# Kernel tuning notes

Hardware: AMD Instinct MI355X
Metric: run time of the kernel (lower is better)

## Reference

```python
import jax, jax.numpy as jnp
import numpy as np

EPS = 1e-12


def _l2norm(v):
    return v / (jnp.linalg.norm(v) + EPS)


def _sn(W, u):
    """One-step power-iteration spectral normalization (torch spectral_norm, 1x1 conv weight).
    W: (out, in), u: (out,). u/v are treated as buffers (no grad)."""
    Wm = W.reshape(W.shape[0], -1)
    v = _l2norm(Wm.T @ u)
    u2 = _l2norm(Wm @ v)
    u2 = jax.lax.stop_gradient(u2)
    v = jax.lax.stop_gradient(v)
    sigma = u2 @ (Wm @ v)
    return W / sigma


def _maxpool2(x):
    # 2x2 max pool, stride 2, NCHW
    N, C, H, W = x.shape
    return x.reshape(N, C, H // 2, 2, W // 2, 2).max(axis=(3, 5))


def setup_inputs() -> dict:
    key = jax.random.key(0)
    ks = jax.random.split(key, 10)
    N, C, H, W = 16, 256, 64, 64
    s = 0.05  # keep logits moderate
    return {
        "x": jax.random.normal(ks[0], (N, C, H, W), dtype=jnp.float32),
        "Wt": jax.random.normal(ks[1], (C >> 3, C), dtype=jnp.float32) * s,
        "Wp": jax.random.normal(ks[2], (C >> 3, C), dtype=jnp.float32) * s,
        "Wg": jax.random.normal(ks[3], (C >> 1, C), dtype=jnp.float32) * s,
        "Wo": jax.random.normal(ks[4], (C, C >> 1), dtype=jnp.float32) * s,
        "ut": jax.random.normal(ks[5], (C >> 3,), dtype=jnp.float32),
        "up": jax.random.normal(ks[6], (C >> 3,), dtype=jnp.float32),
        "ug": jax.random.normal(ks[7], (C >> 1,), dtype=jnp.float32),
        "uo": jax.random.normal(ks[8], (C,), dtype=jnp.float32),
        "gamma": jnp.float32(0.1),  # nonzero so attention branch is exercised
    }


def reference(x, Wt, Wp, Wg, Wo, ut, up, ug, uo, gamma):
    N, C, H, W = x.shape
    L = H * W          # location_num
    Ld = L // 4        # downsampled_num
    # 1x1 convs as channel einsums with spectrally-normalized weights
    theta = jnp.einsum('oc,nchw->nohw', _sn(Wt, ut), x).reshape(N, C >> 3, L)
    phi = _maxpool2(jnp.einsum('oc,nchw->nohw', _sn(Wp, up), x)).reshape(N, C >> 3, Ld)
    attn = jax.nn.softmax(jnp.einsum('ncl,ncm->nlm', theta, phi), axis=-1)  # (N, L, Ld)
    g = _maxpool2(jnp.einsum('oc,nchw->nohw', _sn(Wg, ug), x)).reshape(N, C >> 1, Ld)
    attn_g = jnp.einsum('ncm,nlm->ncl', g, attn).reshape(N, C >> 1, H, W)
    attn_g = jnp.einsum('oc,nchw->nohw', _sn(Wo, uo), attn_g)
    return x + gamma * attn_g
```

## Files before the change

kernel.cpp:

```cpp
#include <hip/hip_runtime.h>
#include <math.h>

#define EPS 1e-12f

typedef unsigned short ushort_t;
typedef __attribute__((ext_vector_type(8))) short short8;
typedef __attribute__((ext_vector_type(4))) float f32x4;
typedef __attribute__((ext_vector_type(4))) unsigned short ushort4v;
typedef __attribute__((ext_vector_type(2))) unsigned int uint2v;
typedef __attribute__((ext_vector_type(4))) unsigned int uint32x4;

#define WS_WB_F 0
#define WS_WO_F 24576
#define WS_TH_F 40960
#define WS_PH_F 1089536
#define WS_G_F  1351680

__device__ __forceinline__ ushort_t f2bf(float f) {
  unsigned int u = __float_as_uint(f);
  u += 0x7fffu + ((u >> 16) & 1u);
  return (ushort_t)(u >> 16);
}
__device__ __forceinline__ float bf2f(ushort_t u) {
  return __uint_as_float(((unsigned int)u) << 16);
}
__device__ __forceinline__ unsigned int pack_bfrh(float lo, float hi) {
  unsigned int a = __float_as_uint(lo) + 0x8000u;
  unsigned int b = __float_as_uint(hi) + 0x8000u;
  return (a >> 16) | (b & 0xffff0000u);
}
__device__ __forceinline__ float exp2_hw(float x) {
  float r;
  asm("v_exp_f32 %0, %1" : "=v"(r) : "v"(x));
  return r;
}

__device__ __forceinline__ float block_reduce_sum(float v, float* red) {
  int t = threadIdx.x;
  red[t] = v;
  __syncthreads();
  #pragma unroll
  for (int s = 128; s > 0; s >>= 1) {
    if (t < s) red[t] += red[t + s];
    __syncthreads();
  }
  float r = red[0];
  __syncthreads();
  return r;
}

__global__ __launch_bounds__(256) void sn_kernel(
    const float* __restrict__ Wt, const float* __restrict__ Wp,
    const float* __restrict__ Wg, const float* __restrict__ Wo,
    const float* __restrict__ ut, const float* __restrict__ up,
    const float* __restrict__ ug, const float* __restrict__ uo,
    float* __restrict__ ws) {
  __shared__ float red[256];
  __shared__ float ub[256];
  __shared__ float vb[256];
  const float* W; const float* u; int O, Ci;
  switch (blockIdx.x) {
    case 0:  W = Wt; u = ut; O = 32;  Ci = 256; break;
    case 1:  W = Wp; u = up; O = 32;  Ci = 256; break;
    case 2:  W = Wg; u = ug; O = 128; Ci = 256; break;
    default: W = Wo; u = uo; O = 256; Ci = 128; break;
  }
  int t = threadIdx.x;
  if (t < O) ub[t] = u[t];
  __syncthreads();
  float tv = 0.f;
  if (t < Ci) {
    for (int o = 0; o < O; o++) tv += W[o * Ci + t] * ub[o];
  }
  float nt2 = block_reduce_sum((t < Ci) ? tv * tv : 0.f, red);
  float ntn = sqrtf(nt2);
  if (t < Ci) vb[t] = tv / (ntn + EPS);
  __syncthreads();
  float sv = 0.f;
  if (t < O) {
    const float* Wr = W + (size_t)t * Ci;
    for (int c = 0; c < Ci; c += 4) {
      float4 wv = *(const float4*)(Wr + c);
      sv += wv.x * vb[c] + wv.y * vb[c + 1] + wv.z * vb[c + 2] + wv.w * vb[c + 3];
    }
  }
  float ss = block_reduce_sum((t < O) ? sv * sv : 0.f, red);
  float ns = sqrtf(ss);
  float sigma = ss / (ns + EPS);
  float inv = 1.f / sigma;
  if (blockIdx.x == 0) inv *= 1.44269504088896f;
  int total = O * Ci;
  if (blockIdx.x == 3) {
    ushort_t* dst = (ushort_t*)(ws + WS_WO_F);
    for (int i = t; i < total; i += 256) {
      int o = i >> 7, c = i & 127;
      int oct = o >> 4, l16o = o & 15, kc = c >> 5, cl = c & 31;
      int kap = (cl < 16) ? ((cl >> 2) * 8 + (cl & 3))
                          : (((cl >> 2) & 3) * 8 + 4 + (cl & 3));
      dst[(((kc * 16 + oct) * 64 + (kap >> 3) * 16 + l16o) << 3) + (kap & 7)] =
          f2bf(W[i] * inv);
    }
  } else {
    int base_row = (blockIdx.x == 0) ? 0 : (blockIdx.x == 1 ? 32 : 64);
    ushort_t* dst = (ushort_t*)(ws + WS_WB_F);
    for (int i = t; i < total; i += 256) {
      int o = i >> 8, c = i & 255;
      int og = base_row + o;
      int mtg = og >> 4, l16o = og & 15, kc = c >> 5, qd = (c >> 3) & 3, j = c & 7;
      dst[(((mtg * 8 + kc) * 64 + qd * 16 + l16o) << 3) + j] = f2bf(W[i] * inv);
    }
  }
}

__global__ __launch_bounds__(256, 2) void proj_mfma(
    const float* __restrict__ x, const ushort_t* __restrict__ wb,
    ushort_t* __restrict__ theta_b, ushort_t* __restrict__ phi_b,
    ushort_t* __restrict__ g_fb) {
  __shared__ ushort_t xb[128 * 264];
  const int t = threadIdx.x;
  const int n = blockIdx.y;
  const int l0 = blockIdx.x * 128;
  const float* xn = x + ((size_t)n * 256) * 4096 + l0;
  {
    const int lrel = t & 127;
    const int half = t >> 7;
    #pragma unroll 4
    for (int ch = 0; ch < 16; ++ch) {
      int chunk = half * 16 + ch;
      short8 v;
      #pragma unroll
      for (int j = 0; j < 8; ++j) {
        float f = xn[(size_t)(chunk * 8 + j) * 4096 + lrel];
        v[j] = (short)f2bf(f);
      }
      *(short8*)(&xb[lrel * 264 + chunk * 8]) = v;
    }
  }
  __syncthreads();
  const int w = t >> 6;
  const int lane = t & 63;
  const int quad = lane >> 4;
  const int l16 = lane & 15;
  const int rowA = (w * 16 + l16) * 264;
  const int rowB = (64 + w * 16 + l16) * 264;
  const int hd = blockIdx.x;
  #pragma unroll 1
  for (int pass = 0; pass < 2; ++pass) {
    f32x4 accA[6], accB[6];
    #pragma unroll
    for (int i = 0; i < 6; ++i) {
      accA[i] = (f32x4){0.f, 0.f, 0.f, 0.f};
      accB[i] = (f32x4){0.f, 0.f, 0.f, 0.f};
    }
    #pragma unroll
    for (int kc = 0; kc < 8; ++kc) {
      short8 bA = *(const short8*)(&xb[rowA + kc * 32 + quad * 8]);
      short8 bB = *(const short8*)(&xb[rowB + kc * 32 + quad * 8]);
      #pragma unroll
      for (int mt = 0; mt < 6; ++mt) {
        int mtg = pass * 6 + mt;
        short8 aW = *(const short8*)(wb + (((size_t)(mtg * 8 + kc) * 64 + lane) << 3));
        accA[mt] = __builtin_amdgcn_mfma_f32_16x16x32_bf16(aW, bA, accA[mt], 0, 0, 0);
        accB[mt] = __builtin_amdgcn_mfma_f32_16x16x32_bf16(aW, bB, accB[mt], 0, 0, 0);
      }
    }
    #pragma unroll
    for (int mt = 0; mt < 6; ++mt) {
      int mtg = pass * 6 + mt;
      if (mtg < 2) {
        int lA = l0 + w * 16 + l16;
        ushort4v vA, vB;
        #pragma unroll
        for (int r = 0; r < 4; ++r) { vA[r] = f2bf(accA[mt][r]); vB[r] = f2bf(accB[mt][r]); }
        *(ushort4v*)(theta_b + ((size_t)n * 4096 + lA) * 32 + mtg * 16 + quad * 4) = vA;
        *(ushort4v*)(theta_b + ((size_t)n * 4096 + lA + 64) * 32 + mtg * 16 + quad * 4) = vB;
      } else {
        float pm[4];
        #pragma unroll
        for (int r = 0; r < 4; ++r) {
          float v = fmaxf(accA[mt][r], accB[mt][r]);
          v = fmaxf(v, __shfl_xor(v, 1));
          pm[r] = v;
        }
        if ((l16 & 1) == 0) {
          int rr = l16 >> 1;
          if (mtg < 4) {
            int mp = hd * 32 + ((rr & 4) ? 16 : 0) + w * 4 + (rr & 3);
            ushort4v vv;
            #pragma unroll
            for (int r = 0; r < 4; ++r) vv[r] = f2bf(pm[r]);
            *(ushort4v*)(phi_b + ((size_t)n * 1024 + mp) * 32 + (mtg - 2) * 16 + quad * 4) = vv;
          } else {
            size_t fb = (size_t)n * 131072 +
                        (size_t)((hd * 8 + (mtg - 4)) * 64 + w * 16 + quad * 4) * 8 + rr;
            #pragma unroll
            for (int r = 0; r < 4; ++r)
              g_fb[fb + (size_t)r * 8] = f2bf(pm[r]);
          }
        }
      }
    }
  }
}

__global__ __launch_bounds__(256, 4) void attn_mfma(
    const float* __restrict__ x,
    const ushort_t* __restrict__ theta_b,
    const ushort_t* __restrict__ phi_b,
    const ushort_t* __restrict__ g_fb,
    const ushort_t* __restrict__ Wo_fb,
    const float* __restrict__ gamma_p,
    float* __restrict__ out) {
  __shared__ ushort_t outb[256 * 68];

  const int t = threadIdx.x;
  const int w = t >> 6;
  const int lane = t & 63;
  const int quad = lane >> 4;
  const int l16 = lane & 15;

  const int flat = blockIdx.y * 64 + blockIdx.x;
  const int nf = ((flat & 7) << 7) | (flat >> 3);
  const int n = nf >> 6;
  const int l0 = (nf & 63) << 6;
  const int lq = l0 + w * 16;

  const short8 bth = *(const short8*)(theta_b + ((size_t)n * 4096 + lq + l16) * 32 + quad * 8);
  const ushort_t* phiN = phi_b + (size_t)n * 1024 * 32;
  const ushort_t* gN   = g_fb + (size_t)n * 131072;

  f32x4 oacc[8];
  #pragma unroll
  for (int j = 0; j < 8; ++j) oacc[j] = (f32x4){0.f, 0.f, 0.f, 0.f};
  float M = -3.0e38f, L = 0.f;

  #pragma unroll 1
  for (int mc = 0; mc < 8; ++mc) {
    const int m0 = mc * 128;
    const f32x4 z = (f32x4){0.f, 0.f, 0.f, 0.f};
    f32x4 st[8];
    #pragma unroll
    for (int i = 0; i < 8; ++i) {
      short8 aph = *(const short8*)(phiN + (size_t)(m0 + i * 16 + l16) * 32 + quad * 8);
      st[i] = __builtin_amdgcn_mfma_f32_16x16x32_bf16(aph, bth, z, 0, 0, 0);
    }
    f32x4 a0 = st[0], a1 = st[1], a2 = st[2], a3 = st[3];
    #pragma unroll
    for (int r = 0; r < 4; ++r) {
      a0[r] = fmaxf(a0[r], st[4][r]); a1[r] = fmaxf(a1[r], st[5][r]);
      a2[r] = fmaxf(a2[r], st[6][r]); a3[r] = fmaxf(a3[r], st[7][r]);
    }
    #pragma unroll
    for (int r = 0; r < 4; ++r) { a0[r] = fmaxf(a0[r], a2[r]); a1[r] = fmaxf(a1[r], a3[r]); }
    float mx = fmaxf(fmaxf(fmaxf(a0[0], a1[0]), fmaxf(a0[1], a1[1])),
                     fmaxf(fmaxf(a0[2], a1[2]), fmaxf(a0[3], a1[3])));
    mx = fmaxf(mx, __shfl_xor(mx, 16));
    mx = fmaxf(mx, __shfl_xor(mx, 32));
    float nm = fmaxf(M, mx);
    float alpha = exp2_hw(M - nm);
    M = nm;
    #pragma unroll
    for (int i = 0; i < 8; ++i) {
      #pragma unroll
      for (int r = 0; r < 4; ++r) st[i][r] = exp2_hw(st[i][r] - nm);
    }
    f32x4 s0 = st[0], s1 = st[1];
    #pragma unroll
    for (int r = 0; r < 4; ++r) {
      s0[r] += st[2][r] + st[4][r] + st[6][r];
      s1[r] += st[3][r] + st[5][r] + st[7][r];
    }
    float ps = (s0[0] + s1[0]) + (s0[1] + s1[1]) + (s0[2] + s1[2]) + (s0[3] + s1[3]);
    L = L * alpha + ps;
    #pragma unroll
    for (int j = 0; j < 8; ++j) {
      #pragma unroll
      for (int r = 0; r < 4; ++r) oacc[j][r] *= alpha;
    }
    unsigned int pk[16];
    #pragma unroll
    for (int i = 0; i < 8; ++i) {
      pk[2 * i]     = pack_bfrh(st[i][0], st[i][1]);
      pk[2 * i + 1] = pack_bfrh(st[i][2], st[i][3]);
    }
    __builtin_amdgcn_s_setprio(1);
    #pragma unroll
    for (int s = 0; s < 4; ++s) {
      uint32x4 u = {pk[4 * s], pk[4 * s + 1], pk[4 * s + 2], pk[4 * s + 3]};
      short8 pb = __builtin_bit_cast(short8, u);
      #pragma unroll
      for (int j = 0; j < 8; ++j) {
        short8 gf = *(const short8*)(gN + (((size_t)((mc * 4 + s) * 8 + j) * 64 + lane) << 3));
        oacc[j] = __builtin_amdgcn_mfma_f32_16x16x32_bf16(gf, pb, oacc[j], 0, 0, 0);
      }
    }
    __builtin_amdgcn_s_setprio(0);
  }

  L += __shfl_xor(L, 16);
  L += __shfl_xor(L, 32);
  const float invL = 1.f / L;
  f32x4 acc2[16];
  #pragma unroll
  for (int i = 0; i < 16; ++i) acc2[i] = (f32x4){0.f, 0.f, 0.f, 0.f};
  #pragma unroll
  for (int kc = 0; kc < 4; ++kc) {
    uint32x4 u;
    u[0] = pack_bfrh(oacc[2 * kc][0] * invL, oacc[2 * kc][1] * invL);
    u[1] = pack_bfrh(oacc[2 * kc][2] * invL, oacc[2 * kc][3] * invL);
    u[2] = pack_bfrh(oacc[2 * kc + 1][0] * invL, oacc[2 * kc + 1][1] * invL);
    u[3] = pack_bfrh(oacc[2 * kc + 1][2] * invL, oacc[2 * kc + 1][3] * invL);
    short8 aO = __builtin_bit_cast(short8, u);
    #pragma unroll
    for (int oct = 0; oct < 16; ++oct) {
      short8 bw = *(const short8*)(Wo_fb + (((size_t)(kc * 16 + oct) * 64 + lane) << 3));
      acc2[oct] = __builtin_amdgcn_mfma_f32_16x16x32_bf16(aO, bw, acc2[oct], 0, 0, 0);
    }
  }
  #pragma unroll
  for (int oct = 0; oct < 16; ++oct) {
    uint2v p2;
    p2[0] = pack_bfrh(acc2[oct][0], acc2[oct][1]);
    p2[1] = pack_bfrh(acc2[oct][2], acc2[oct][3]);
    *(uint2v*)(&outb[(oct * 16 + l16) * 68 + w * 16 + quad * 4]) = p2;
  }
  __syncthreads();
  {
    const float gm = gamma_p[0];
    const int oc = (t >> 4);
    const int lch = (t & 15) * 4;
    #pragma unroll
    for (int ocg = 0; ocg < 16; ++ocg) {
      int row = ocg * 16 + oc;
      ushort4v ov = *(const ushort4v*)(&outb[row * 68 + lch]);
      const float* xp = x + ((size_t)n * 256 + row) * 4096 + l0 + lch;
      float* op = out + ((size_t)n * 256 + row) * 4096 + l0 + lch;
      float4 xv = *(const float4*)xp;
      float4 v;
      v.x = xv.x + gm * bf2f(ov[0]);
      v.y = xv.y + gm * bf2f(ov[1]);
      v.z = xv.z + gm * bf2f(ov[2]);
      v.w = xv.w + gm * bf2f(ov[3]);
      *(float4*)op = v;
    }
  }
}

extern "C" void kernel_launch(void* const* d_in, const int* in_sizes, int n_in,
                              void* d_out, int out_size, void* d_ws, size_t ws_size,
                              hipStream_t stream) {
  const float* x  = (const float*)d_in[0];
  const float* Wt = (const float*)d_in[1];
  const float* Wp = (const float*)d_in[2];
  const float* Wg = (const float*)d_in[3];
  const float* Wo = (const float*)d_in[4];
  const float* ut = (const float*)d_in[5];
  const float* up = (const float*)d_in[6];
  const float* ug = (const float*)d_in[7];
  const float* uo = (const float*)d_in[8];
  const float* gamma = (const float*)d_in[9];
  float* ws  = (float*)d_ws;
  float* out = (float*)d_out;

  ushort_t* wb      = (ushort_t*)(ws + WS_WB_F);
  ushort_t* Wo_b    = (ushort_t*)(ws + WS_WO_F);
  ushort_t* theta_b = (ushort_t*)(ws + WS_TH_F);
  ushort_t* phi_b   = (ushort_t*)(ws + WS_PH_F);
  ushort_t* g_fb    = (ushort_t*)(ws + WS_G_F);

  sn_kernel<<<4, 256, 0, stream>>>(Wt, Wp, Wg, Wo, ut, up, ug, uo, ws);
  proj_mfma<<<dim3(32, 16), 256, 0, stream>>>(x, wb, theta_b, phi_b, g_fb);
  attn_mfma<<<dim3(64, 16), 256, 0, stream>>>(x, theta_b, phi_b, g_fb, Wo_b, gamma, out);
}
```

Baseline: 224.6 us.

## Stage g chunks into LDS via async global_load_lds, shared across waves

Measured after the change: 204.9 us. 1.1x faster.

```diff
diff --git a/kernel.cpp b/kernel.cpp
--- a/kernel.cpp
+++ b/kernel.cpp
@@ -33,6 +33,12 @@
   float r;
   asm("v_exp_f32 %0, %1" : "=v"(r) : "v"(x));
   return r;
+}
+
+__device__ __forceinline__ void gload_lds16(const ushort_t* g, ushort_t* l) {
+  __builtin_amdgcn_global_load_lds(
+      (const __attribute__((address_space(1))) unsigned int*)g,
+      (__attribute__((address_space(3))) unsigned int*)l, 16, 0, 0);
 }
 
 __device__ __forceinline__ float block_reduce_sum(float v, float* red) {
@@ -211,7 +217,9 @@
     const ushort_t* __restrict__ Wo_fb,
     const float* __restrict__ gamma_p,
     float* __restrict__ out) {
-  __shared__ ushort_t outb[256 * 68];
+  __shared__ __align__(16) unsigned char smem[34816];
+  ushort_t* gbuf = (ushort_t*)smem;
+  ushort_t* outb = (ushort_t*)smem;
 
   const int t = threadIdx.x;
   const int w = t >> 6;
@@ -233,9 +241,17 @@
   #pragma unroll
   for (int j = 0; j < 8; ++j) oacc[j] = (f32x4){0.f, 0.f, 0.f, 0.f};
   float M = -3.0e38f, L = 0.f;
-
-  #pragma unroll 1
-  for (int mc = 0; mc < 8; ++mc) {
+  unsigned int pk[16];
+
+  auto STAGE = [&](int mc) {
+    const ushort_t* src = gN + (size_t)mc * 16384 + w * 8 * 512 + lane * 8;
+    ushort_t* dst = gbuf + w * 8 * 512;
+    #pragma unroll
+    for (int b = 0; b < 8; ++b)
+      gload_lds16(src + b * 512, dst + b * 512);
+  };
+
+  auto QKSM = [&](int mc) {
     const int m0 = mc * 128;
     const f32x4 z = (f32x4){0.f, 0.f, 0.f, 0.f};
     f32x4 st[8];
@@ -277,12 +293,14 @@
       #pragma unroll
       for (int r = 0; r < 4; ++r) oacc[j][r] *= alpha;
     }
-    unsigned int pk[16];
     #pragma unroll
     for (int i = 0; i < 8; ++i) {
       pk[2 * i]     = pack_bfrh(st[i][0], st[i][1]);
       pk[2 * i + 1] = pack_bfrh(st[i][2], st[i][3]);
     }
+  };
+
+  auto PV = [&]() {
     __builtin_amdgcn_s_setprio(1);
     #pragma unroll
     for (int s = 0; s < 4; ++s) {
@@ -290,39 +308,59 @@
       short8 pb = __builtin_bit_cast(short8, u);
       #pragma unroll
       for (int j = 0; j < 8; ++j) {
-        short8 gf = *(const short8*)(gN + (((size_t)((mc * 4 + s) * 8 + j) * 64 + lane) << 3));
+        short8 gf = *(const short8*)(gbuf + (size_t)(s * 8 + j) * 512 + lane * 8);
         oacc[j] = __builtin_amdgcn_mfma_f32_16x16x32_bf16(gf, pb, oacc[j], 0, 0, 0);
       }
     }
     __builtin_amdgcn_s_setprio(0);
-  }
+  };
+
+  STAGE(0);
+  QKSM(0);
+  __syncthreads();
+  #pragma unroll 1
+  for (int mc = 0; mc < 8; ++mc) {
+    PV();
+    if (mc < 7) {
+      __syncthreads();
+      STAGE(mc + 1);
+      QKSM(mc + 1);
+      __syncthreads();
+    }
+  }
+  __syncthreads();
 
   L += __shfl_xor(L, 16);
   L += __shfl_xor(L, 32);
   const float invL = 1.f / L;
-  f32x4 acc2[16];
   #pragma unroll
-  for (int i = 0; i < 16; ++i) acc2[i] = (f32x4){0.f, 0.f, 0.f, 0.f};
-  #pragma unroll
-  for (int kc = 0; kc < 4; ++kc) {
-    uint32x4 u;
-    u[0] = pack_bfrh(oacc[2 * kc][0] * invL, oacc[2 * kc][1] * invL);
-    u[1] = pack_bfrh(oacc[2 * kc][2] * invL, oacc[2 * kc][3] * invL);
-    u[2] = pack_bfrh(oacc[2 * kc + 1][0] * invL, oacc[2 * kc + 1][1] * invL);
-    u[3] = pack_bfrh(oacc[2 * kc + 1][2] * invL, oacc[2 * kc + 1][3] * invL);
-    short8 aO = __builtin_bit_cast(short8, u);
-    #pragma unroll
-    for (int oct = 0; oct < 16; ++oct) {
-      short8 bw = *(const short8*)(Wo_fb + (((size_t)(kc * 16 + oct) * 64 + lane) << 3));
-      acc2[oct] = __builtin_amdgcn_mfma_f32_16x16x32_bf16(aO, bw, acc2[oct], 0, 0, 0);
-    }
-  }
-  #pragma unroll
-  for (int oct = 0; oct < 16; ++oct) {
-    uint2v p2;
-    p2[0] = pack_bfrh(acc2[oct][0], acc2[oct][1]);
-    p2[1] = pack_bfrh(acc2[oct][2], acc2[oct][3]);
-    *(uint2v*)(&outb[(oct * 16 + l16) * 68 + w * 16 + quad * 4]) = p2;
+  for (int half = 0; half < 2; ++half) {
+    f32x4 acc2[8];
+    #pragma unroll
+    for (int i = 0; i < 8; ++i) acc2[i] = (f32x4){0.f, 0.f, 0.f, 0.f};
+    #pragma unroll
+    for (int kc = 0; kc < 4; ++kc) {
+      uint32x4 u;
+      u[0] = pack_bfrh(oacc[2 * kc][0] * invL, oacc[2 * kc][1] * invL);
+      u[1] = pack_bfrh(oacc[2 * kc][2] * invL, oacc[2 * kc][3] * invL);
+      u[2] = pack_bfrh(oacc[2 * kc + 1][0] * invL, oacc[2 * kc + 1][1] * invL);
+      u[3] = pack_bfrh(oacc[2 * kc + 1][2] * invL, oacc[2 * kc + 1][3] * invL);
+      short8 aO = __builtin_bit_cast(short8, u);
+      #pragma unroll
+      for (int o8 = 0; o8 < 8; ++o8) {
+        int oct = half * 8 + o8;
+        short8 bw = *(const short8*)(Wo_fb + (((size_t)(kc * 16 + oct) * 64 + lane) << 3));
+        acc2[o8] = __builtin_amdgcn_mfma_f32_16x16x32_bf16(aO, bw, acc2[o8], 0, 0, 0);
+      }
+    }
+    #pragma unroll
+    for (int o8 = 0; o8 < 8; ++o8) {
+      int oct = half * 8 + o8;
+      uint2v p2;
+      p2[0] = pack_bfrh(acc2[o8][0], acc2[o8][1]);
+      p2[1] = pack_bfrh(acc2[o8][2], acc2[o8][3]);
+      *(uint2v*)(&outb[(oct * 16 + l16) * 68 + w * 16 + quad * 4]) = p2;
+    }
   }
   __syncthreads();
   {
```
